# Kernel tuning notes

Hardware: AMD Instinct MI355X
Metric: run time of the kernel (lower is better)

## Reference

```python
import jax, jax.numpy as jnp
import numpy as np

N_NODES = 50000
N_EDGES = 1_600_000
DIMS = [3, 4096, 1024, 256, 64, 16]  # conv1..conv5 in/out widths


def setup_inputs() -> dict:
    key = jax.random.key(0)
    ks = jax.random.split(key, 2 + 2 * 6)
    x = jax.random.normal(ks[0], (N_NODES, DIMS[0]), jnp.float32)
    edge_index = jax.random.randint(ks[1], (2, N_EDGES), 0, N_NODES, jnp.int64)
    inp = {"x": x, "edge_index": edge_index}
    # GCNConv weights (lin has no bias fused; bias added after aggregation)
    for i in range(5):
        fi, fo = DIMS[i], DIMS[i + 1]
        inp[f"W{i+1}"] = jax.random.normal(ks[2 + 2 * i], (fi, fo), jnp.float32) / np.float32(np.sqrt(fi))
        inp[f"b{i+1}"] = jnp.zeros((fo,), jnp.float32)
    # final Linear(num_classes, 3)
    inp["Wl"] = jax.random.normal(ks[12], (DIMS[5], 3), jnp.float32) / np.float32(np.sqrt(DIMS[5]))
    inp["bl"] = jnp.zeros((3,), jnp.float32)
    return inp


def _gcn_layer(x, W, b, src, dst, dinv):
    """GCNConv: h = XW; out = D^-1/2 (A+I) D^-1/2 h + b (self-loops included)."""
    h = x @ W  # [N, out]
    norm = dinv[src] * dinv[dst]  # [E]
    agg = jax.ops.segment_sum(h[src] * norm[:, None], dst, num_segments=N_NODES)
    # self-loop term: norm_ii = dinv[i]^2
    return agg + h * (dinv * dinv)[:, None] + b


def reference(x, edge_index, W1, b1, W2, b2, W3, b3, W4, b4, W5, b5, Wl, bl):
    src, dst = edge_index[0], edge_index[1]
    # degree with self-loops (edge weights = 1), computed on target nodes
    deg = jax.ops.segment_sum(jnp.ones((N_EDGES,), x.dtype), dst, num_segments=N_NODES) + 1.0
    dinv = jax.lax.rsqrt(deg)
    h = _gcn_layer(x, W1, b1, src, dst, dinv)
    h = jax.nn.relu(h)  # dropout = identity in eval
    h = _gcn_layer(h, W2, b2, src, dst, dinv)
    h = jax.nn.relu(h)
    h = _gcn_layer(h, W3, b3, src, dst, dinv)
    h = jax.nn.relu(h)
    h = _gcn_layer(h, W4, b4, src, dst, dinv)
    h = jax.nn.relu(h)
    h = _gcn_layer(h, W5, b5, src, dst, dinv)
    # scatter_mean with broadcast index [0] -> global mean pool to [1, C]
    pooled = jnp.mean(h, axis=0, keepdims=True)
    return pooled @ Wl + bl  # [1, 3]
```

## Files before the change

### kernel.cpp

```cpp
#include <hip/hip_runtime.h>
#include <stdint.h>

#define NN 50000
#define NE 1600000

typedef _Float16 f16;
typedef __attribute__((ext_vector_type(8))) _Float16 h8;
typedef __attribute__((ext_vector_type(4))) _Float16 h4v;
typedef __attribute__((ext_vector_type(4))) float f32x4;
typedef __attribute__((ext_vector_type(2))) float f32x2;

union PackU { unsigned int u; f16 h[2]; };
union Pack4 { uint2 v; f16 h[4]; };
union Pack8 { uint4 v; f16 h[8]; };

__device__ __forceinline__ void storev(float* p, float v) { *p = v; }
__device__ __forceinline__ void storev(f16* p, float v) { *p = (f16)v; }

__device__ __forceinline__ unsigned char f2fp8(float v) {
    int pk = __builtin_amdgcn_cvt_pk_fp8_f32(v, v, 0, false);
    return (unsigned char)(pk & 0xff);
}

__global__ __launch_bounds__(256) void zero_int_kernel(int* __restrict__ p, int n) {
    int i = blockIdx.x * 256 + threadIdx.x;
    if (i < n) p[i] = 0;
}

__global__ __launch_bounds__(256) void count_kernel(const int* __restrict__ dst,
                                                    int* __restrict__ deg, int nE) {
    int e = blockIdx.x * 256 + threadIdx.x;
    if (e < nE) atomicAdd(&deg[dst[e]], 1);
}

__global__ __launch_bounds__(256) void dinv_kernel(const int* __restrict__ deg,
                                                   float* __restrict__ dinv, int n) {
    int i = blockIdx.x * 256 + threadIdx.x;
    if (i < n) dinv[i] = rsqrtf((float)deg[i] + 1.0f);
}

__global__ __launch_bounds__(256) void scan1_kernel(const int* __restrict__ cnt,
                                                    int* __restrict__ rs,
                                                    int* __restrict__ bsum, int n) {
    __shared__ int sm[256];
    int b = blockIdx.x, t = threadIdx.x, i = b * 256 + t;
    int v = (i < n) ? cnt[i] : 0;
    sm[t] = v;
    __syncthreads();
    for (int off = 1; off < 256; off <<= 1) {
        int x = 0;
        if (t >= off) x = sm[t - off];
        __syncthreads();
        if (t >= off) sm[t] += x;
        __syncthreads();
    }
    if (i < n) rs[i] = sm[t] - v;
    if (t == 255) bsum[b] = sm[255];
}

__global__ __launch_bounds__(256) void scan2_kernel(int* __restrict__ bsum,
                                                    int* __restrict__ rs, int nb, int n) {
    __shared__ int sm[256];
    int t = threadIdx.x;
    int v = (t < nb) ? bsum[t] : 0;
    sm[t] = v;
    __syncthreads();
    for (int off = 1; off < 256; off <<= 1) {
        int x = 0;
        if (t >= off) x = sm[t - off];
        __syncthreads();
        if (t >= off) sm[t] += x;
        __syncthreads();
    }
    if (t < nb) bsum[t] = sm[t] - v;
    if (t == 255) rs[n] = sm[255];
}

__global__ __launch_bounds__(256) void scan3_kernel(int* __restrict__ rs,
                                                    const int* __restrict__ bsum, int n) {
    int i = blockIdx.x * 256 + threadIdx.x;
    if (i < n) rs[i] += bsum[blockIdx.x];
}

__global__ __launch_bounds__(256) void fill_kernel(const int* __restrict__ src,
                                                   const int* __restrict__ dst,
                                                   const int* __restrict__ rs,
                                                   int* __restrict__ cur,
                                                   int* __restrict__ csr, int nE) {
    int e = blockIdx.x * 256 + threadIdx.x;
    if (e < nE) {
        int d = dst[e];
        int p = rs[d] + atomicAdd(&cur[d], 1);
        csr[p] = src[e];
    }
}

__global__ __launch_bounds__(256) void pack_w1_kernel(const float* __restrict__ W1,
                                                      const float* __restrict__ b1,
                                                      float* __restrict__ w1p) {
    int k = blockIdx.x * 256 + threadIdx.x;
    if (k < 4096) {
        w1p[k * 4 + 0] = W1[k];
        w1p[k * 4 + 1] = W1[4096 + k];
        w1p[k * 4 + 2] = W1[8192 + k];
        w1p[k * 4 + 3] = b1[k];
    }
}

__global__ __launch_bounds__(256) void tconv_kernel(const float* __restrict__ W,
                                                    f16* __restrict__ Wt,
                                                    int K, int N) {
    __shared__ float tile[32][33];
    int kb = blockIdx.y * 32, nb = blockIdx.x * 32;
    int tx = threadIdx.x & 31, ty = threadIdx.x >> 5;
    for (int r = ty; r < 32; r += 8)
        tile[r][tx] = W[(size_t)(kb + r) * N + nb + tx];
    __syncthreads();
    for (int r = ty; r < 32; r += 8)
        Wt[(size_t)(nb + r) * K + kb + tx] = (f16)tile[tx][r];
}

template <int F, int TPN, bool RELU, bool BIAS, typename OutT>
__global__ __launch_bounds__(256) void agg_kernel(const float* __restrict__ t,
                                                  const float* __restrict__ dinv,
                                                  const int* __restrict__ rs,
                                                  const int* __restrict__ csr,
                                                  const float* __restrict__ bias,
                                                  OutT* __restrict__ out, int out_ld,
                                                  int nNodes) {
    constexpr int NPB = 256 / TPN;
    constexpr int C   = F / TPN;
    static_assert(TPN * C == F, "F must be TPN*C");
    int node = blockIdx.x * NPB + (int)threadIdx.x / TPN;
    if (node >= nNodes) return;
    int lane = (int)threadIdx.x % TPN;

    float acc[C];
#pragma unroll
    for (int c = 0; c < C; ++c) acc[c] = 0.f;

    int e0 = rs[node], e1 = rs[node + 1];
    for (int e = e0; e < e1; ++e) {
        int s = csr[e];
        float w = dinv[s];
        const float* tr = t + (size_t)s * F;
#pragma unroll
        for (int c = 0; c < C; ++c) acc[c] += w * tr[lane + c * TPN];
    }
    float di = dinv[node];
    const float* ti = t + (size_t)node * F;
    OutT* oi = out + (size_t)node * out_ld;
#pragma unroll
    for (int c = 0; c < C; ++c) {
        int col = lane + c * TPN;
        float v = di * acc[c] + di * di * ti[col];
        if (BIAS) v += bias[col];
        if (RELU) v = fmaxf(v, 0.f);
        storev(oi + col, v);
    }
}

template <bool RELU>
__global__ __launch_bounds__(256) void agg_fp8_1024(const unsigned char* __restrict__ t,
                                                    const float* __restrict__ dinv,
                                                    const int* __restrict__ rs,
                                                    const int* __restrict__ csr,
                                                    const float* __restrict__ bias,
                                                    f16* __restrict__ out, int nNodes) {
    int node = blockIdx.x * 4 + ((int)threadIdx.x >> 6);
    if (node >= nNodes) return;
    int lane = (int)threadIdx.x & 63;

    float acc[16];
#pragma unroll
    for (int j = 0; j < 16; ++j) acc[j] = 0.f;

    int e0 = rs[node], e1 = rs[node + 1];
    int e = e0;
    for (; e + 1 < e1; e += 2) {
        int s0 = csr[e], s1 = csr[e + 1];
        float w0 = dinv[s0], w1 = dinv[s1];
        uint4 u0 = ((const uint4*)(t + (size_t)s0 * 1024))[lane];
        uint4 u1 = ((const uint4*)(t + (size_t)s1 * 1024))[lane];
        const unsigned int uw0[4] = {u0.x, u0.y, u0.z, u0.w};
        const unsigned int uw1[4] = {u1.x, u1.y, u1.z, u1.w};
#pragma unroll
        for (int q = 0; q < 4; ++q) {
            f32x2 l0 = __builtin_amdgcn_cvt_pk_f32_fp8((int)uw0[q], false);
            f32x2 h0 = __builtin_amdgcn_cvt_pk_f32_fp8((int)uw0[q], true);
            f32x2 l1 = __builtin_amdgcn_cvt_pk_f32_fp8((int)uw1[q], false);
            f32x2 h1 = __builtin_amdgcn_cvt_pk_f32_fp8((int)uw1[q], true);
            acc[q * 4 + 0] += w0 * l0.x + w1 * l1.x;
            acc[q * 4 + 1] += w0 * l0.y + w1 * l1.y;
            acc[q * 4 + 2] += w0 * h0.x + w1 * h1.x;
            acc[q * 4 + 3] += w0 * h0.y + w1 * h1.y;
        }
    }
    if (e < e1) {
        int s0 = csr[e];
        float w0 = dinv[s0];
        uint4 u0 = ((const uint4*)(t + (size_t)s0 * 1024))[lane];
        const unsigned int uw0[4] = {u0.x, u0.y, u0.z, u0.w};
#pragma unroll
        for (int q = 0; q < 4; ++q) {
            f32x2 l0 = __builtin_amdgcn_cvt_pk_f32_fp8((int)uw0[q], false);
            f32x2 h0 = __builtin_amdgcn_cvt_pk_f32_fp8((int)uw0[q], true);
            acc[q * 4 + 0] += w0 * l0.x;
            acc[q * 4 + 1] += w0 * l0.y;
            acc[q * 4 + 2] += w0 * h0.x;
            acc[q * 4 + 3] += w0 * h0.y;
        }
    }
    float di = dinv[node], di2 = di * di;
    uint4 us = ((const uint4*)(t + (size_t)node * 1024))[lane];
    const unsigned int uws[4] = {us.x, us.y, us.z, us.w};
    Pack8 o0, o1;
#pragma unroll
    for (int q = 0; q < 4; ++q) {
        f32x2 sl = __builtin_amdgcn_cvt_pk_f32_fp8((int)uws[q], false);
        f32x2 sh = __builtin_amdgcn_cvt_pk_f32_fp8((int)uws[q], true);
        float4 b = *(const float4*)(bias + 16 * lane + q * 4);
        float v0 = di * acc[q * 4 + 0] + di2 * sl.x + b.x;
        float v1 = di * acc[q * 4 + 1] + di2 * sl.y + b.y;
        float v2 = di * acc[q * 4 + 2] + di2 * sh.x + b.z;
        float v3 = di * acc[q * 4 + 3] + di2 * sh.y + b.w;
        if (RELU) {
            v0 = fmaxf(v0, 0.f); v1 = fmaxf(v1, 0.f);
            v2 = fmaxf(v2, 0.f); v3 = fmaxf(v3, 0.f);
        }
        Pack8& dst8 = (q < 2) ? o0 : o1;
        int base = (q & 1) * 4;
        dst8.h[base + 0] = (f16)v0;
        dst8.h[base + 1] = (f16)v1;
        dst8.h[base + 2] = (f16)v2;
        dst8.h[base + 3] = (f16)v3;
    }
    uint4* orow = (uint4*)(out + (size_t)node * 1024 + 16 * lane);
    orow[0] = o0.v;
    orow[1] = o1.v;
}

template <bool RELU>
__global__ __launch_bounds__(256) void agg_fp8_256(const unsigned char* __restrict__ t,
                                                   int in_ld,
                                                   const float* __restrict__ dinv,
                                                   const int* __restrict__ rs,
                                                   const int* __restrict__ csr,
                                                   const float* __restrict__ bias,
                                                   f16* __restrict__ out,
                                                   int out_ld, int nNodes) {
    int node = blockIdx.x * 4 + ((int)threadIdx.x >> 6);
    if (node >= nNodes) return;
    int lane = (int)threadIdx.x & 63;

    float acc0 = 0.f, acc1 = 0.f, acc2 = 0.f, acc3 = 0.f;
    int e0 = rs[node], e1 = rs[node + 1];
    int e = e0;
    for (; e + 1 < e1; e += 2) {
        int s0 = csr[e], s1 = csr[e + 1];
        float w0 = dinv[s0], w1 = dinv[s1];
        unsigned int u0 = ((const unsigned int*)(t + (size_t)s0 * in_ld))[lane];
        unsigned int u1 = ((const unsigned int*)(t + (size_t)s1 * in_ld))[lane];
        f32x2 l0 = __builtin_amdgcn_cvt_pk_f32_fp8((int)u0, false);
        f32x2 h0 = __builtin_amdgcn_cvt_pk_f32_fp8((int)u0, true);
        f32x2 l1 = __builtin_amdgcn_cvt_pk_f32_fp8((int)u1, false);
        f32x2 h1 = __builtin_amdgcn_cvt_pk_f32_fp8((int)u1, true);
        acc0 += w0 * l0.x + w1 * l1.x;
        acc1 += w0 * l0.y + w1 * l1.y;
        acc2 += w0 * h0.x + w1 * h1.x;
        acc3 += w0 * h0.y + w1 * h1.y;
    }
    if (e < e1) {
        int s0 = csr[e];
        float w0 = dinv[s0];
        unsigned int u0 = ((const unsigned int*)(t + (size_t)s0 * in_ld))[lane];
        f32x2 l0 = __builtin_amdgcn_cvt_pk_f32_fp8((int)u0, false);
        f32x2 h0 = __builtin_amdgcn_cvt_pk_f32_fp8((int)u0, true);
        acc0 += w0 * l0.x;
        acc1 += w0 * l0.y;
        acc2 += w0 * h0.x;
        acc3 += w0 * h0.y;
    }
    float di = dinv[node], di2 = di * di;
    unsigned int us = ((const unsigned int*)(t + (size_t)node * in_ld))[lane];
    f32x2 sl = __builtin_amdgcn_cvt_pk_f32_fp8((int)us, false);
    f32x2 sh = __builtin_amdgcn_cvt_pk_f32_fp8((int)us, true);
    float4 b = *(const float4*)(bias + 4 * lane);
    float v0 = di * acc0 + di2 * sl.x + b.x;
    float v1 = di * acc1 + di2 * sl.y + b.y;
    float v2 = di * acc2 + di2 * sh.x + b.z;
    float v3 = di * acc3 + di2 * sh.y + b.w;
    if (RELU) {
        v0 = fmaxf(v0, 0.f); v1 = fmaxf(v1, 0.f);
        v2 = fmaxf(v2, 0.f); v3 = fmaxf(v3, 0.f);
    }
    Pack4 pk;
    pk.h[0] = (f16)v0; pk.h[1] = (f16)v1; pk.h[2] = (f16)v2; pk.h[3] = (f16)v3;
    *(uint2*)(out + (size_t)node * out_ld + 4 * lane) = pk.v;
}

#define LDSTR 40

__global__ __launch_bounds__(512, 4) void gemm12_mfma4(const float* __restrict__ aggx,
                                                       const float* __restrict__ w1p,
                                                       const f16* __restrict__ Bt,
                                                       unsigned char* __restrict__ t2) {
    __shared__ f16 As[128 * LDSTR] __attribute__((aligned(16)));
    __shared__ f16 Bs[256 * LDSTR] __attribute__((aligned(16)));
    int tid = threadIdx.x;
    int m0  = blockIdx.x * 128;
    int n0c = blockIdx.y * 256;

    int mg = tid >> 3;
    int kg = tid & 7;
    float a0[2], a1[2], a2[2];
#pragma unroll
    for (int j = 0; j < 2; ++j) {
        int gm = m0 + mg * 2 + j;
        if (gm < NN) {
            a0[j] = aggx[gm * 3 + 0];
            a1[j] = aggx[gm * 3 + 1];
            a2[j] = aggx[gm * 3 + 2];
        } else {
            a0[j] = a1[j] = a2[j] = 0.f;
        }
    }

    int brow = tid >> 1;
    int bkof = (tid & 1) * 16;
    const f16* bbase = Bt + (size_t)(n0c + brow) * 4096 + bkof;

    int lane   = tid & 63;
    int wv     = tid >> 6;
    int wm     = (wv >> 2) * 64;
    int wn     = (wv & 3) * 64;
    int fr_m   = lane & 15;
    int khalf8 = (lane >> 4) * 8;

    h8 pb0 = *(const h8*)(bbase);
    h8 pb1 = *(const h8*)(bbase + 8);

    f32x4 acc[4][4];
#pragma unroll
    for (int i = 0; i < 4; ++i)
#pragma unroll
        for (int j = 0; j < 4; ++j) acc[i][j] = (f32x4){0.f, 0.f, 0.f, 0.f};

    for (int k0 = 0; k0 < 4096; k0 += 32) {
        int kb = k0 + kg * 4;
        float4 wk0 = *(const float4*)(w1p + (size_t)(kb + 0) * 4);
        float4 wk1 = *(const float4*)(w1p + (size_t)(kb + 1) * 4);
        float4 wk2 = *(const float4*)(w1p + (size_t)(kb + 2) * 4);
        float4 wk3 = *(const float4*)(w1p + (size_t)(kb + 3) * 4);
#pragma unroll
        for (int j = 0; j < 2; ++j) {
            float h0 = fmaxf(a0[j] * wk0.x + a1[j] * wk0.y + a2[j] * wk0.z + wk0.w, 0.f);
            float h1 = fmaxf(a0[j] * wk1.x + a1[j] * wk1.y + a2[j] * wk1.z + wk1.w, 0.f);
            float h2 = fmaxf(a0[j] * wk2.x + a1[j] * wk2.y + a2[j] * wk2.z + wk2.w, 0.f);
            float h3 = fmaxf(a0[j] * wk3.x + a1[j] * wk3.y + a2[j] * wk3.z + wk3.w, 0.f);
            Pack4 pk;
            pk.h[0] = (f16)h0; pk.h[1] = (f16)h1; pk.h[2] = (f16)h2; pk.h[3] = (f16)h3;
            *(uint2*)(&As[(mg * 2 + j) * LDSTR + kg * 4]) = pk.v;
        }
        *(h8*)(&Bs[brow * LDSTR + bkof]) = pb0;
        *(h8*)(&Bs[brow * LDSTR + bkof + 8]) = pb1;
        __syncthreads();

        int kn = k0 + 32;
        if (kn < 4096) {
            pb0 = *(const h8*)(bbase + kn);
            pb1 = *(const h8*)(bbase + kn + 8);
        }

        h8 af[4];
#pragma unroll
        for (int mt = 0; mt < 4; ++mt)
            af[mt] = *(const h8*)(&As[(wm + mt * 16 + fr_m) * LDSTR + khalf8]);
#pragma unroll
        for (int nt = 0; nt < 4; ++nt) {
            h8 bf = *(const h8*)(&Bs[(wn + nt * 16 + fr_m) * LDSTR + khalf8]);
#pragma unroll
            for (int mt = 0; mt < 4; ++mt)
                acc[mt][nt] = __builtin_amdgcn_mfma_f32_16x16x32_f16(af[mt], bf, acc[mt][nt], 0, 0, 0);
        }
        __syncthreads();
    }

#pragma unroll
    for (int mt = 0; mt < 4; ++mt) {
#pragma unroll
        for (int reg = 0; reg < 4; ++reg) {
            int gm = m0 + wm + mt * 16 + (lane >> 4) * 4 + reg;
            if (gm < NN) {
                unsigned char* orow = t2 + (size_t)gm * 1024 + n0c + wn + fr_m;
#pragma unroll
                for (int nt = 0; nt < 4; ++nt)
                    orow[nt * 16] = f2fp8(acc[mt][nt][reg]);
            }
        }
    }
}

__global__ __launch_bounds__(256) void gemm_mfma(const f16* __restrict__ A, int lda,
                                                 const f16* __restrict__ Bt, int K,
                                                 unsigned char* __restrict__ C, int ldc,
                                                 int M) {
    __shared__ f16 As[128 * LDSTR] __attribute__((aligned(16)));
    __shared__ f16 Bs[128 * LDSTR] __attribute__((aligned(16)));
    int tid = threadIdx.x;
    int m0 = blockIdx.y * 128;
    int n0 = blockIdx.x * 128;

    int row = tid >> 1;
    int kof = (tid & 1) * 16;
    int am  = m0 + row;
    if (am > M - 1) am = M - 1;

    int lane   = tid & 63;
    int wv     = tid >> 6;
    int fr_m   = lane & 15;
    int khalf8 = (lane >> 4) * 8;

    const f16* abase = A + (size_t)am * lda + kof;
    const f16* bbase = Bt + (size_t)(n0 + row) * K + kof;

    h8 pa0 = *(const h8*)(abase);
    h8 pa1 = *(const h8*)(abase + 8);
    h8 pb0 = *(const h8*)(bbase);
    h8 pb1 = *(const h8*)(bbase + 8);

    f32x4 acc[2][8];
#pragma unroll
    for (int i = 0; i < 2; ++i)
#pragma unroll
        for (int j = 0; j < 8; ++j) acc[i][j] = (f32x4){0.f, 0.f, 0.f, 0.f};

    for (int k0 = 0; k0 < K; k0 += 32) {
        *(h8*)(&As[row * LDSTR + kof]) = pa0;
        *(h8*)(&As[row * LDSTR + kof + 8]) = pa1;
        *(h8*)(&Bs[row * LDSTR + kof]) = pb0;
        *(h8*)(&Bs[row * LDSTR + kof + 8]) = pb1;
        __syncthreads();

        int kn = k0 + 32;
        if (kn < K) {
            pa0 = *(const h8*)(abase + kn);
            pa1 = *(const h8*)(abase + kn + 8);
            pb0 = *(const h8*)(bbase + kn);
            pb1 = *(const h8*)(bbase + kn + 8);
        }

        h8 af0 = *(const h8*)(&As[(wv * 32 + fr_m) * LDSTR + khalf8]);
        h8 af1 = *(const h8*)(&As[(wv * 32 + 16 + fr_m) * LDSTR + khalf8]);
#pragma unroll
        for (int nt = 0; nt < 8; ++nt) {
            h8 bf = *(const h8*)(&Bs[(nt * 16 + fr_m) * LDSTR + khalf8]);
            acc[0][nt] = __builtin_amdgcn_mfma_f32_16x16x32_f16(af0, bf, acc[0][nt], 0, 0, 0);
            acc[1][nt] = __builtin_amdgcn_mfma_f32_16x16x32_f16(af1, bf, acc[1][nt], 0, 0, 0);
        }
        __syncthreads();
    }

#pragma unroll
    for (int mt = 0; mt < 2; ++mt) {
#pragma unroll
        for (int reg = 0; reg < 4; ++reg) {
            int gm = m0 + wv * 32 + mt * 16 + (lane >> 4) * 4 + reg;
            if (gm < M) {
                unsigned char* orow = C + (size_t)gm * ldc + n0 + fr_m;
#pragma unroll
                for (int nt = 0; nt < 8; ++nt)
                    orow[nt * 16] = f2fp8(acc[mt][nt][reg]);
            }
        }
    }
}

#define BM 64
#define BN 64
#define BKS 16
__global__ __launch_bounds__(256) void gemm_f16A_kernel(const f16* __restrict__ A,
                                                        const float* __restrict__ B,
                                                        float* __restrict__ C,
                                                        int M, int K, int N) {
    __shared__ float As[BKS][BM + 4];
    __shared__ float Bs[BKS][BN + 4];
    int tid = threadIdx.x;
    int tx = tid & 15;
    int ty = tid >> 4;
    int m0 = blockIdx.y * BM;
    int n0 = blockIdx.x * BN;

    float acc[4][4];
#pragma unroll
    for (int i = 0; i < 4; ++i)
#pragma unroll
        for (int j = 0; j < 4; ++j) acc[i][j] = 0.f;

    int lmA = tid >> 2;
    int lkA = (tid & 3) * 4;
    int lkB = tid >> 4;
    int lnB = (tid & 15) * 4;

    for (int k0 = 0; k0 < K; k0 += BKS) {
        int gm = m0 + lmA;
        if (gm > M - 1) gm = M - 1;
        h4v av = *(const h4v*)(A + (size_t)gm * K + k0 + lkA);
        As[lkA + 0][lmA] = (float)av.x;
        As[lkA + 1][lmA] = (float)av.y;
        As[lkA + 2][lmA] = (float)av.z;
        As[lkA + 3][lmA] = (float)av.w;
        float4 bv = *reinterpret_cast<const float4*>(B + (size_t)(k0 + lkB) * N + n0 + lnB);
        *reinterpret_cast<float4*>(&Bs[lkB][lnB]) = bv;
        __syncthreads();

#pragma unroll
        for (int k = 0; k < BKS; ++k) {
            float4 a4 = *reinterpret_cast<const float4*>(&As[k][ty * 4]);
            float4 b4 = *reinterpret_cast<const float4*>(&Bs[k][tx * 4]);
            float a[4] = {a4.x, a4.y, a4.z, a4.w};
            float b[4] = {b4.x, b4.y, b4.z, b4.w};
#pragma unroll
            for (int i = 0; i < 4; ++i)
#pragma unroll
                for (int j = 0; j < 4; ++j) acc[i][j] += a[i] * b[j];
        }
        __syncthreads();
    }

#pragma unroll
    for (int i = 0; i < 4; ++i) {
        int m = m0 + ty * 4 + i;
        if (m < M) {
            float4 o = make_float4(acc[i][0], acc[i][1], acc[i][2], acc[i][3]);
            *reinterpret_cast<float4*>(C + (size_t)m * N + n0 + tx * 4) = o;
        }
    }
}

__global__ __launch_bounds__(256) void gemm5_kernel(const f16* __restrict__ h4,
                                                    const float* __restrict__ W5,
                                                    float* __restrict__ t5, int nNodes) {
    int idx = blockIdx.x * 256 + threadIdx.x;
    int i = idx >> 4, j = idx & 15;
    if (i >= nNodes) return;
    const f16* a = h4 + (size_t)i * 64;
    float s = 0.f;
#pragma unroll
    for (int k = 0; k < 64; ++k) s += (float)a[k] * W5[k * 16 + j];
    t5[idx] = s;
}

__global__ __launch_bounds__(256) void pool_kernel(const float* __restrict__ h5,
                                                   float* __restrict__ pool) {
    __shared__ float red[256];
    int c = blockIdx.x;
    float s = 0.f;
    for (int i = threadIdx.x; i < NN; i += 256) s += h5[(size_t)i * 16 + c];
    red[threadIdx.x] = s;
    __syncthreads();
    for (int off = 128; off > 0; off >>= 1) {
        if ((int)threadIdx.x < off) red[threadIdx.x] += red[threadIdx.x + off];
        __syncthreads();
    }
    if (threadIdx.x == 0) pool[c] = red[0];
}

__global__ void final_kernel(const float* __restrict__ pool, const float* __restrict__ Wl,
                             const float* __restrict__ bl, float* __restrict__ out) {
    int j = threadIdx.x;
    if (j < 3) {
        float s = 0.f;
#pragma unroll
        for (int c = 0; c < 16; ++c) s += pool[c] * Wl[c * 3 + j];
        out[j] = s * (1.0f / (float)NN) + bl[j];
    }
}

extern "C" void kernel_launch(void* const* d_in, const int* in_sizes, int n_in,
                              void* d_out, int out_size, void* d_ws, size_t ws_size,
                              hipStream_t stream) {
    (void)in_sizes; (void)n_in; (void)out_size; (void)ws_size;

    const float* x  = (const float*)d_in[0];
    const int*   ei = (const int*)d_in[1];
    const float* W1 = (const float*)d_in[2];
    const float* b1 = (const float*)d_in[3];
    const float* W2 = (const float*)d_in[4];
    const float* b2 = (const float*)d_in[5];
    const float* W3 = (const float*)d_in[6];
    const float* b3 = (const float*)d_in[7];
    const float* W4 = (const float*)d_in[8];
    const float* b4 = (const float*)d_in[9];
    const float* W5 = (const float*)d_in[10];
    const float* b5 = (const float*)d_in[11];
    const float* Wl = (const float*)d_in[12];
    const float* bl = (const float*)d_in[13];
    float* out = (float*)d_out;

    const int* srcp = ei;
    const int* dstp = ei + NE;

    char* p = (char*)d_ws;
    auto carve = [&](size_t bytes) {
        char* r = p;
        p += (bytes + 255) & ~(size_t)255;
        return r;
    };
    int*   deg  = (int*)carve(NN * 4);
    int*   cur  = (int*)carve(NN * 4);
    int*   rs   = (int*)carve((NN + 1) * 4);
    int*   bsum = (int*)carve(256 * 4);
    int*   csr  = (int*)carve((size_t)NE * 4);
    float* dinv = (float*)carve(NN * 4);
    float* aggx = (float*)carve((size_t)NN * 3 * 4);
    float* pool = (float*)carve(16 * 4);
    float* w1p  = (float*)carve((size_t)4096 * 4 * 4);
    f16*   w2t  = (f16*)carve((size_t)1024 * 4096 * 2);
    f16*   w3t  = (f16*)carve((size_t)256 * 1024 * 2);
    unsigned char* tbuf = (unsigned char*)carve((size_t)NN * 1024);
    f16*   h2   = (f16*)carve((size_t)NN * 1024 * 2);
    f16*   h3   = (f16*)carve((size_t)NN * 256 * 2);
    f16*   h4   = (f16*)carve((size_t)NN * 64 * 2);
    float* h5   = (float*)carve((size_t)NN * 16 * 4);
    float* tf32 = (float*)tbuf;

    const int NB = (NN + 255) / 256;

    zero_int_kernel<<<NB, 256, 0, stream>>>(deg, NN);
    zero_int_kernel<<<NB, 256, 0, stream>>>(cur, NN);
    count_kernel<<<(NE + 255) / 256, 256, 0, stream>>>(dstp, deg, NE);
    dinv_kernel<<<NB, 256, 0, stream>>>(deg, dinv, NN);
    scan1_kernel<<<NB, 256, 0, stream>>>(deg, rs, bsum, NN);
    scan2_kernel<<<1, 256, 0, stream>>>(bsum, rs, NB, NN);
    scan3_kernel<<<NB, 256, 0, stream>>>(rs, bsum, NN);
    fill_kernel<<<(NE + 255) / 256, 256, 0, stream>>>(srcp, dstp, rs, cur, csr, NE);

    pack_w1_kernel<<<16, 256, 0, stream>>>(W1, b1, w1p);
    tconv_kernel<<<dim3(1024 / 32, 4096 / 32), 256, 0, stream>>>(W2, w2t, 4096, 1024);
    tconv_kernel<<<dim3(256 / 32, 1024 / 32), 256, 0, stream>>>(W3, w3t, 1024, 256);

    agg_kernel<3, 1, false, false, float><<<NB, 256, 0, stream>>>(
        x, dinv, rs, csr, nullptr, aggx, 3, NN);

    const int MB2 = (NN + 127) / 128;

    gemm12_mfma4<<<dim3(MB2, 4), 512, 0, stream>>>(aggx, w1p, w2t, tbuf);
    agg_fp8_1024<true><<<(NN + 3) / 4, 256, 0, stream>>>(
        tbuf, dinv, rs, csr, b2, h2, NN);

    gemm_mfma<<<dim3(2, MB2), 256, 0, stream>>>(
        h2, 1024, w3t, 1024, tbuf, 256, NN);
    agg_fp8_256<true><<<(NN + 3) / 4, 256, 0, stream>>>(
        tbuf, 256, dinv, rs, csr, b3, h3, 256, NN);

    gemm_f16A_kernel<<<dim3(1, (NN + BM - 1) / BM), 256, 0, stream>>>(
        h3, W4, tf32, NN, 256, 64);
    agg_kernel<64, 64, true, true, f16><<<(NN + 3) / 4, 256, 0, stream>>>(
        tf32, dinv, rs, csr, b4, h4, 64, NN);

    gemm5_kernel<<<(NN * 16 + 255) / 256, 256, 0, stream>>>(h4, W5, tf32, NN);
    agg_kernel<16, 16, false, true, float><<<(NN + 15) / 16, 256, 0, stream>>>(
        tf32, dinv, rs, csr, b5, h5, 16, NN);

    pool_kernel<<<16, 256, 0, stream>>>(h5, pool);
    final_kernel<<<1, 64, 0, stream>>>(pool, Wl, bl, out);
}
```

Before: 1.635 ms.

## Double-buffer LDS tiles in fused layer-1/2 GEMM to drop one barrier per step

The fused GEMM kernel now keeps two LDS buffers for the A and B tiles. The next tile is written into the alternate buffer while MFMAs read the current one, and the W1 loads are prefetched a step ahead, so each k-step needs one barrier instead of two. The cost is double the shared memory and a lower occupancy hint in launch_bounds (2 instead of 4), which could reduce latency hiding.

```diff
diff --git a/kernel.cpp b/kernel.cpp
--- a/kernel.cpp
+++ b/kernel.cpp
@@ -301,12 +301,12 @@
 
 #define LDSTR 40
 
-__global__ __launch_bounds__(512, 4) void gemm12_mfma4(const float* __restrict__ aggx,
+__global__ __launch_bounds__(512, 2) void gemm12_mfma6(const float* __restrict__ aggx,
                                                        const float* __restrict__ w1p,
                                                        const f16* __restrict__ Bt,
                                                        unsigned char* __restrict__ t2) {
-    __shared__ f16 As[128 * LDSTR] __attribute__((aligned(16)));
-    __shared__ f16 Bs[256 * LDSTR] __attribute__((aligned(16)));
+    __shared__ f16 As[2][128 * LDSTR] __attribute__((aligned(16)));
+    __shared__ f16 Bs[2][256 * LDSTR] __attribute__((aligned(16)));
     int tid = threadIdx.x;
     int m0  = blockIdx.x * 128;
     int n0c = blockIdx.y * 256;
@@ -337,54 +337,73 @@
     int fr_m   = lane & 15;
     int khalf8 = (lane >> 4) * 8;
 
+    f32x4 acc[4][4];
+#pragma unroll
+    for (int i = 0; i < 4; ++i)
+#pragma unroll
+        for (int j = 0; j < 4; ++j) acc[i][j] = (f32x4){0.f, 0.f, 0.f, 0.f};
+
+#define STAGE_WRITE(bufi, wk0, wk1, wk2, wk3, pb0, pb1)                          \
+    {                                                                            \
+        _Pragma("unroll")                                                        \
+        for (int j = 0; j < 2; ++j) {                                            \
+            float h0 = fmaxf(a0[j] * wk0.x + a1[j] * wk0.y + a2[j] * wk0.z + wk0.w, 0.f); \
+            float h1 = fmaxf(a0[j] * wk1.x + a1[j] * wk1.y + a2[j] * wk1.z + wk1.w, 0.f); \
+            float h2 = fmaxf(a0[j] * wk2.x + a1[j] * wk2.y + a2[j] * wk2.z + wk2.w, 0.f); \
+            float h3 = fmaxf(a0[j] * wk3.x + a1[j] * wk3.y + a2[j] * wk3.z + wk3.w, 0.f); \
+            Pack4 pk;                                                            \
+            pk.h[0] = (f16)h0; pk.h[1] = (f16)h1;                                \
+            pk.h[2] = (f16)h2; pk.h[3] = (f16)h3;                                \
+            *(uint2*)(&As[bufi][(mg * 2 + j) * LDSTR + kg * 4]) = pk.v;          \
+        }                                                                        \
+        *(h8*)(&Bs[bufi][brow * LDSTR + bkof]) = pb0;                            \
+        *(h8*)(&Bs[bufi][brow * LDSTR + bkof + 8]) = pb1;                        \
+    }
+
     h8 pb0 = *(const h8*)(bbase);
     h8 pb1 = *(const h8*)(bbase + 8);
-
-    f32x4 acc[4][4];
-#pragma unroll
-    for (int i = 0; i < 4; ++i)
-#pragma unroll
-        for (int j = 0; j < 4; ++j) acc[i][j] = (f32x4){0.f, 0.f, 0.f, 0.f};
-
-    for (int k0 = 0; k0 < 4096; k0 += 32) {
-        int kb = k0 + kg * 4;
-        float4 wk0 = *(const float4*)(w1p + (size_t)(kb + 0) * 4);
-        float4 wk1 = *(const float4*)(w1p + (size_t)(kb + 1) * 4);
-        float4 wk2 = *(const float4*)(w1p + (size_t)(kb + 2) * 4);
-        float4 wk3 = *(const float4*)(w1p + (size_t)(kb + 3) * 4);
-#pragma unroll
-        for (int j = 0; j < 2; ++j) {
-            float h0 = fmaxf(a0[j] * wk0.x + a1[j] * wk0.y + a2[j] * wk0.z + wk0.w, 0.f);
-            float h1 = fmaxf(a0[j] * wk1.x + a1[j] * wk1.y + a2[j] * wk1.z + wk1.w, 0.f);
-            float h2 = fmaxf(a0[j] * wk2.x + a1[j] * wk2.y + a2[j] * wk2.z + wk2.w, 0.f);
-            float h3 = fmaxf(a0[j] * wk3.x + a1[j] * wk3.y + a2[j] * wk3.z + wk3.w, 0.f);
-            Pack4 pk;
-            pk.h[0] = (f16)h0; pk.h[1] = (f16)h1; pk.h[2] = (f16)h2; pk.h[3] = (f16)h3;
-            *(uint2*)(&As[(mg * 2 + j) * LDSTR + kg * 4]) = pk.v;
-        }
-        *(h8*)(&Bs[brow * LDSTR + bkof]) = pb0;
-        *(h8*)(&Bs[brow * LDSTR + bkof + 8]) = pb1;
-        __syncthreads();
-
-        int kn = k0 + 32;
-        if (kn < 4096) {
-            pb0 = *(const h8*)(bbase + kn);
-            pb1 = *(const h8*)(bbase + kn + 8);
-        }
-
+    float4 w0v = *(const float4*)(w1p + (size_t)(kg * 4 + 0) * 4);
+    float4 w1v = *(const float4*)(w1p + (size_t)(kg * 4 + 1) * 4);
+    float4 w2v = *(const float4*)(w1p + (size_t)(kg * 4 + 2) * 4);
+    float4 w3v = *(const float4*)(w1p + (size_t)(kg * 4 + 3) * 4);
+    STAGE_WRITE(0, w0v, w1v, w2v, w3v, pb0, pb1);
+    __syncthreads();
+    pb0 = *(const h8*)(bbase + 32);
+    pb1 = *(const h8*)(bbase + 40);
+    w0v = *(const float4*)(w1p + (size_t)(32 + kg * 4 + 0) * 4);
+    w1v = *(const float4*)(w1p + (size_t)(32 + kg * 4 + 1) * 4);
+    w2v = *(const float4*)(w1p + (size_t)(32 + kg * 4 + 2) * 4);
+    w3v = *(const float4*)(w1p + (size_t)(32 + kg * 4 + 3) * 4);
+
+    for (int i = 0; i < 128; ++i) {
+        int buf = i & 1;
         h8 af[4];
 #pragma unroll
         for (int mt = 0; mt < 4; ++mt)
-            af[mt] = *(const h8*)(&As[(wm + mt * 16 + fr_m) * LDSTR + khalf8]);
+            af[mt] = *(const h8*)(&As[buf][(wm + mt * 16 + fr_m) * LDSTR + khalf8]);
 #pragma unroll
         for (int nt = 0; nt < 4; ++nt) {
-            h8 bf = *(const h8*)(&Bs[(wn + nt * 16 + fr_m) * LDSTR + khalf8]);
+            h8 bf = *(const h8*)(&Bs[buf][(wn + nt * 16 + fr_m) * LDSTR + khalf8]);
 #pragma unroll
             for (int mt = 0; mt < 4; ++mt)
                 acc[mt][nt] = __builtin_amdgcn_mfma_f32_16x16x32_f16(af[mt], bf, acc[mt][nt], 0, 0, 0);
         }
-        __syncthreads();
-    }
+        if (i + 1 < 128) {
+            STAGE_WRITE(buf ^ 1, w0v, w1v, w2v, w3v, pb0, pb1);
+            __syncthreads();
+            if (i + 2 < 128) {
+                int kb = (i + 2) * 32;
+                pb0 = *(const h8*)(bbase + kb);
+                pb1 = *(const h8*)(bbase + kb + 8);
+                int kk = kb + kg * 4;
+                w0v = *(const float4*)(w1p + (size_t)(kk + 0) * 4);
+                w1v = *(const float4*)(w1p + (size_t)(kk + 1) * 4);
+                w2v = *(const float4*)(w1p + (size_t)(kk + 2) * 4);
+                w3v = *(const float4*)(w1p + (size_t)(kk + 3) * 4);
+            }
+        }
+    }
+#undef STAGE_WRITE
 
 #pragma unroll
     for (int mt = 0; mt < 4; ++mt) {
@@ -645,7 +664,7 @@
 
     const int MB2 = (NN + 127) / 128;
 
-    gemm12_mfma4<<<dim3(MB2, 4), 512, 0, stream>>>(aggx, w1p, w2t, tbuf);
+    gemm12_mfma6<<<dim3(MB2, 4), 512, 0, stream>>>(aggx, w1p, w2t, tbuf);
     agg_fp8_1024<true><<<(NN + 3) / 4, 256, 0, stream>>>(
         tbuf, dinv, rs, csr, b2, h2, NN);
 
```

After: 1.916 ms. +17.2%, slower.

## Unfuse layer-1 activation from layer-2 GEMM using chunked materialized h1

Applied to the files above, without the earlier changes.

Removes the fused gemm12 kernel, which recomputed relu(aggx·W1+b1) inside the GEMM main loop. Layer-1 activations are now written to an f16 scratch buffer (reusing h2 memory) in four row chunks of 12500, and each chunk is multiplied by W2 with the generic gemm_mfma kernel. The aim is to take the per-tile elementwise work and the w1p loads out of the MFMA loop and reuse the plain GEMM kernel. The cost is roughly 100MB of extra f16 writes and reads per pass plus eight extra launches.

```diff
diff --git a/kernel.cpp b/kernel.cpp
--- a/kernel.cpp
+++ b/kernel.cpp
@@ -118,6 +118,29 @@
     __syncthreads();
     for (int r = ty; r < 32; r += 8)
         Wt[(size_t)(nb + r) * K + kb + tx] = (f16)tile[tx][r];
+}
+
+__global__ __launch_bounds__(256) void h1_kernel(const float* __restrict__ aggx,
+                                                 const float* __restrict__ w1p,
+                                                 f16* __restrict__ h1c,
+                                                 int r0, int rows) {
+    int k2 = blockIdx.x * 512 + (int)threadIdx.x * 2;
+    float4 wA = *(const float4*)(w1p + (size_t)k2 * 4);
+    float4 wB = *(const float4*)(w1p + (size_t)(k2 + 1) * 4);
+    int rbase = blockIdx.y * 16;
+#pragma unroll 4
+    for (int rr = 0; rr < 16; ++rr) {
+        int r = rbase + rr;
+        if (r >= rows) break;
+        int gr = r0 + r;
+        float a0 = aggx[gr * 3 + 0], a1 = aggx[gr * 3 + 1], a2 = aggx[gr * 3 + 2];
+        float hA = fmaxf(a0 * wA.x + a1 * wA.y + a2 * wA.z + wA.w, 0.f);
+        float hB = fmaxf(a0 * wB.x + a1 * wB.y + a2 * wB.z + wB.w, 0.f);
+        PackU pw;
+        pw.h[0] = (f16)hA;
+        pw.h[1] = (f16)hB;
+        *(unsigned int*)(h1c + (size_t)r * 4096 + k2) = pw.u;
+    }
 }
 
 template <int F, int TPN, bool RELU, bool BIAS, typename OutT>
@@ -300,106 +323,6 @@
 }
 
 #define LDSTR 40
-
-__global__ __launch_bounds__(512, 4) void gemm12_mfma4(const float* __restrict__ aggx,
-                                                       const float* __restrict__ w1p,
-                                                       const f16* __restrict__ Bt,
-                                                       unsigned char* __restrict__ t2) {
-    __shared__ f16 As[128 * LDSTR] __attribute__((aligned(16)));
-    __shared__ f16 Bs[256 * LDSTR] __attribute__((aligned(16)));
-    int tid = threadIdx.x;
-    int m0  = blockIdx.x * 128;
-    int n0c = blockIdx.y * 256;
-
-    int mg = tid >> 3;
-    int kg = tid & 7;
-    float a0[2], a1[2], a2[2];
-#pragma unroll
-    for (int j = 0; j < 2; ++j) {
-        int gm = m0 + mg * 2 + j;
-        if (gm < NN) {
-            a0[j] = aggx[gm * 3 + 0];
-            a1[j] = aggx[gm * 3 + 1];
-            a2[j] = aggx[gm * 3 + 2];
-        } else {
-            a0[j] = a1[j] = a2[j] = 0.f;
-        }
-    }
-
-    int brow = tid >> 1;
-    int bkof = (tid & 1) * 16;
-    const f16* bbase = Bt + (size_t)(n0c + brow) * 4096 + bkof;
-
-    int lane   = tid & 63;
-    int wv     = tid >> 6;
-    int wm     = (wv >> 2) * 64;
-    int wn     = (wv & 3) * 64;
-    int fr_m   = lane & 15;
-    int khalf8 = (lane >> 4) * 8;
-
-    h8 pb0 = *(const h8*)(bbase);
-    h8 pb1 = *(const h8*)(bbase + 8);
-
-    f32x4 acc[4][4];
-#pragma unroll
-    for (int i = 0; i < 4; ++i)
-#pragma unroll
-        for (int j = 0; j < 4; ++j) acc[i][j] = (f32x4){0.f, 0.f, 0.f, 0.f};
-
-    for (int k0 = 0; k0 < 4096; k0 += 32) {
-        int kb = k0 + kg * 4;
-        float4 wk0 = *(const float4*)(w1p + (size_t)(kb + 0) * 4);
-        float4 wk1 = *(const float4*)(w1p + (size_t)(kb + 1) * 4);
-        float4 wk2 = *(const float4*)(w1p + (size_t)(kb + 2) * 4);
-        float4 wk3 = *(const float4*)(w1p + (size_t)(kb + 3) * 4);
-#pragma unroll
-        for (int j = 0; j < 2; ++j) {
-            float h0 = fmaxf(a0[j] * wk0.x + a1[j] * wk0.y + a2[j] * wk0.z + wk0.w, 0.f);
-            float h1 = fmaxf(a0[j] * wk1.x + a1[j] * wk1.y + a2[j] * wk1.z + wk1.w, 0.f);
-            float h2 = fmaxf(a0[j] * wk2.x + a1[j] * wk2.y + a2[j] * wk2.z + wk2.w, 0.f);
-            float h3 = fmaxf(a0[j] * wk3.x + a1[j] * wk3.y + a2[j] * wk3.z + wk3.w, 0.f);
-            Pack4 pk;
-            pk.h[0] = (f16)h0; pk.h[1] = (f16)h1; pk.h[2] = (f16)h2; pk.h[3] = (f16)h3;
-            *(uint2*)(&As[(mg * 2 + j) * LDSTR + kg * 4]) = pk.v;
-        }
-        *(h8*)(&Bs[brow * LDSTR + bkof]) = pb0;
-        *(h8*)(&Bs[brow * LDSTR + bkof + 8]) = pb1;
-        __syncthreads();
-
-        int kn = k0 + 32;
-        if (kn < 4096) {
-            pb0 = *(const h8*)(bbase + kn);
-            pb1 = *(const h8*)(bbase + kn + 8);
-        }
-
-        h8 af[4];
-#pragma unroll
-        for (int mt = 0; mt < 4; ++mt)
-            af[mt] = *(const h8*)(&As[(wm + mt * 16 + fr_m) * LDSTR + khalf8]);
-#pragma unroll
-        for (int nt = 0; nt < 4; ++nt) {
-            h8 bf = *(const h8*)(&Bs[(wn + nt * 16 + fr_m) * LDSTR + khalf8]);
-#pragma unroll
-            for (int mt = 0; mt < 4; ++mt)
-                acc[mt][nt] = __builtin_amdgcn_mfma_f32_16x16x32_f16(af[mt], bf, acc[mt][nt], 0, 0, 0);
-        }
-        __syncthreads();
-    }
-
-#pragma unroll
-    for (int mt = 0; mt < 4; ++mt) {
-#pragma unroll
-        for (int reg = 0; reg < 4; ++reg) {
-            int gm = m0 + wm + mt * 16 + (lane >> 4) * 4 + reg;
-            if (gm < NN) {
-                unsigned char* orow = t2 + (size_t)gm * 1024 + n0c + wn + fr_m;
-#pragma unroll
-                for (int nt = 0; nt < 4; ++nt)
-                    orow[nt * 16] = f2fp8(acc[mt][nt][reg]);
-            }
-        }
-    }
-}
 
 __global__ __launch_bounds__(256) void gemm_mfma(const f16* __restrict__ A, int lda,
                                                  const f16* __restrict__ Bt, int K,
@@ -624,6 +547,7 @@
     f16*   h4   = (f16*)carve((size_t)NN * 64 * 2);
     float* h5   = (float*)carve((size_t)NN * 16 * 4);
     float* tf32 = (float*)tbuf;
+    f16*   h1c  = h2;
 
     const int NB = (NN + 255) / 256;
 
@@ -645,7 +569,13 @@
 
     const int MB2 = (NN + 127) / 128;
 
-    gemm12_mfma4<<<dim3(MB2, 4), 512, 0, stream>>>(aggx, w1p, w2t, tbuf);
+    const int CH = 12500;
+    for (int c = 0; c < 4; ++c) {
+        int r0 = c * CH;
+        h1_kernel<<<dim3(8, (CH + 15) / 16), 256, 0, stream>>>(aggx, w1p, h1c, r0, CH);
+        gemm_mfma<<<dim3(8, (CH + 127) / 128), 256, 0, stream>>>(
+            h1c, 4096, w2t, 4096, tbuf + (size_t)r0 * 1024, 1024, CH);
+    }
     agg_fp8_1024<true><<<(NN + 3) / 4, 256, 0, stream>>>(
         tbuf, dinv, rs, csr, b2, h2, NN);
 
```

Measured after the change: 1.858 ms. 13.6% more time.
